# Kernel tuning notes

Hardware: AMD Instinct MI355X
Metric: run time of the kernel (lower is better)

## Reference

```python
import jax, jax.numpy as jnp
import numpy as np

B, N, D, H = 2, 2048, 512, 8
DH = D  # head_subspaces=False -> d_head = d_model
F = H * DH  # 4096, projected feature dim (RoPE applied over this full dim)


def rotate_half(x):
    # interleaved pairs (lucidrains rotary-embedding-torch default): (x0,x1)->(-x1,x0)
    x2 = x.reshape(*x.shape[:-1], -1, 2)
    return jnp.stack([-x2[..., 1], x2[..., 0]], axis=-1).reshape(x.shape)


def apply_rope(x, cos, sin):
    # x: [B,N,F], cos/sin: [N,F]
    return x * cos[None] + rotate_half(x) * sin[None]


def setup_inputs() -> dict:
    key = jax.random.key(0)
    kx, kq, kk, kv, ko = jax.random.split(key, 5)
    x = jax.random.normal(kx, (B, N, D), dtype=jnp.float32)
    # rotary tables over full projected dim, freqs repeated in interleaved pairs
    inv_freq = 1.0 / (10000.0 ** (jnp.arange(0, F, 2, dtype=jnp.float32) / F))
    freqs = jnp.arange(N, dtype=jnp.float32)[:, None] * inv_freq[None, :]  # [N, F/2]
    freqs = jnp.repeat(freqs, 2, axis=-1)  # [N, F], pairwise interleaved
    cos, sin = jnp.cos(freqs), jnp.sin(freqs)
    # causal bool mask [B, query, target] (3-dim branch of the module)
    target_mask = jnp.broadcast_to(jnp.tril(jnp.ones((N, N), dtype=bool))[None], (B, N, N))
    s = 0.02
    Wq = jax.random.normal(kq, (D, F), dtype=jnp.float32) * s
    Wk = jax.random.normal(kk, (D, F), dtype=jnp.float32) * s
    Wv = jax.random.normal(kv, (D, F), dtype=jnp.float32) * s
    bv = jnp.zeros((F,), dtype=jnp.float32)
    Wo = jax.random.normal(ko, (D, D), dtype=jnp.float32) * s
    bo = jnp.zeros((D,), dtype=jnp.float32)
    return {"x": x, "cos": cos, "sin": sin, "target_mask": target_mask,
            "Wq": Wq, "Wk": Wk, "Wv": Wv, "bv": bv, "Wo": Wo, "bo": bo}


def reference(x, cos, sin, target_mask, Wq, Wk, Wv, bv, Wo, bo):
    b, n, d = x.shape
    Q = apply_rope(x @ Wq, cos, sin)  # RoPE on full [B,N,F] projection
    K = apply_rope(x @ Wk, cos, sin)
    V = x @ Wv + bv
    # split heads: [B,H,N,DH]
    Q = Q.reshape(b, n, H, DH).transpose(0, 2, 1, 3)
    K = K.reshape(b, n, H, DH).transpose(0, 2, 1, 3)
    V = V.reshape(b, n, H, DH).transpose(0, 2, 1, 3)
    A = jnp.einsum('bhid,bhjd->bhij', Q, K)  # NOTE: no 1/sqrt(d) scaling, as in source
    A = jnp.where(target_mask[:, None, :, :], A, -jnp.inf)
    A = jax.nn.softmax(A, axis=-1)
    y = jnp.einsum('bhij,bhjd->bhid', A, V)
    # head_subspaces=False: merge heads by SUM over head axis -> [B,N,D]
    y = y.sum(axis=1)
    y = y * jax.nn.sigmoid(1.702 * y)  # QuickGELU
    return y @ Wo + bo
```

## Files before the change

kernel.cpp:

```cpp
#include <hip/hip_runtime.h>

typedef unsigned short u16;
typedef u16 u16x8 __attribute__((ext_vector_type(8)));
typedef __bf16 bf16x8 __attribute__((ext_vector_type(8)));
typedef float f32x4 __attribute__((ext_vector_type(4)));

#define DEV __device__ __forceinline__
#define MFMA16 __builtin_amdgcn_mfma_f32_16x16x32_bf16

constexpr int Bb = 2, Nctx = 2048, Dm = 512, Hh = 8, Dh = 512, Ff = 4096;
constexpr int Mrows = Bb * Nctx;

DEV float b2f(u16 u) { unsigned int i = ((unsigned int)u) << 16; return __builtin_bit_cast(float, i); }
DEV u16 f2b(float f) {
  unsigned int x = __builtin_bit_cast(unsigned int, f);
  return (u16)((x + 0x7FFFu + ((x >> 16) & 1u)) >> 16);
}
DEV bf16x8 ld8(const u16* p) { return __builtin_bit_cast(bf16x8, *(const u16x8*)p); }

DEV void gload16(const u16* g, u16* l) {
#if defined(__has_builtin) && __has_builtin(__builtin_amdgcn_global_load_lds)
  __builtin_amdgcn_global_load_lds((const __attribute__((address_space(1))) void*)(g),
                                   (__attribute__((address_space(3))) void*)(l), 16, 0, 0);
#else
  *(u16x8*)l = *(const u16x8*)g;
#endif
}

__global__ void convert_k(const float* __restrict__ in, u16* __restrict__ out, int n8) {
  int idx = blockIdx.x * 256 + threadIdx.x;
  if (idx >= n8) return;
  size_t e0 = (size_t)idx * 8;
  f32x4 a = *(const f32x4*)(in + e0);
  f32x4 b = *(const f32x4*)(in + e0 + 4);
  u16x8 o;
  #pragma unroll
  for (int i = 0; i < 4; ++i) { o[i] = f2b(a[i]); o[4 + i] = f2b(b[i]); }
  *(u16x8*)(out + e0) = o;
}

__global__ void transpose_k(const float* __restrict__ in, u16* __restrict__ out,
                            int rows, int cols) {
  __shared__ float tile[32][33];
  int bx = blockIdx.x * 32, by = blockIdx.y * 32;
  int tx = threadIdx.x, ty = threadIdx.y;
  #pragma unroll
  for (int i = ty; i < 32; i += 8)
    tile[i][tx] = in[(size_t)(by + i) * cols + bx + tx];
  __syncthreads();
  #pragma unroll
  for (int i = ty; i < 32; i += 8)
    out[(size_t)(bx + i) * rows + by + tx] = f2b(tile[tx][i]);
}

__global__ void vtrans_k(const u16* __restrict__ V, u16* __restrict__ Vt) {
  __shared__ u16 tile[32][33];
  int z = blockIdx.z;
  int b = z >> 3, h = z & 7;
  int n0 = blockIdx.x * 32, d0 = blockIdx.y * 32;
  int tx = threadIdx.x, ty = threadIdx.y;
  #pragma unroll
  for (int i = ty; i < 32; i += 8)
    tile[i][tx] = V[((size_t)(b * Nctx + n0 + i)) * Ff + h * Dh + d0 + tx];
  __syncthreads();
  #pragma unroll
  for (int i = ty; i < 32; i += 8)
    Vt[((size_t)(z * Dh + d0 + i)) * Nctx + n0 + tx] = tile[tx][i];
}

template <int MODE>
__launch_bounds__(256, 4)
__global__ void gemm2_k(const u16* __restrict__ A, const u16* __restrict__ BT,
                        void* __restrict__ Cout, const float* __restrict__ bias,
                        const float* __restrict__ cs, const float* __restrict__ sn,
                        int Ndim, int Kdim) {
  __shared__ u16 sA[128 * 32];
  __shared__ u16 sB[128 * 32];
  const int tid = threadIdx.x;
  const int wave = tid >> 6, lane = tid & 63, quad = lane >> 4, l16 = lane & 15;
  const int wy = wave >> 1, wx = wave & 1;
  const int m0 = blockIdx.y * 128, n0 = blockIdx.x * 128;
  f32x4 acc[4][4];
  #pragma unroll
  for (int i = 0; i < 4; ++i)
    #pragma unroll
    for (int j = 0; j < 4; ++j)
      #pragma unroll
      for (int r = 0; r < 4; ++r) acc[i][j][r] = 0.f;
  const int srow = tid >> 2, sch = (tid & 3) * 8;
  const u16* agp = A + (size_t)(m0 + srow) * Kdim + sch;
  const u16* bgp = BT + (size_t)(n0 + srow) * Kdim + sch;
  for (int k0 = 0; k0 < Kdim; k0 += 32) {
    __syncthreads();
    gload16(agp + k0, &sA[srow * 32 + sch]);
    gload16(agp + (size_t)64 * Kdim + k0, &sA[(64 + srow) * 32 + sch]);
    gload16(bgp + k0, &sB[srow * 32 + sch]);
    gload16(bgp + (size_t)64 * Kdim + k0, &sB[(64 + srow) * 32 + sch]);
    __syncthreads();
    bf16x8 af[4], bf[4];
    #pragma unroll
    for (int t = 0; t < 4; ++t) af[t] = ld8(&sA[(wy * 64 + t * 16 + l16) * 32 + quad * 8]);
    #pragma unroll
    for (int t = 0; t < 4; ++t) bf[t] = ld8(&sB[(wx * 64 + t * 16 + l16) * 32 + quad * 8]);
    #pragma unroll
    for (int i = 0; i < 4; ++i)
      #pragma unroll
      for (int j = 0; j < 4; ++j)
        acc[i][j] = MFMA16(af[i], bf[j], acc[i][j], 0, 0, 0);
  }
  #pragma unroll
  for (int i = 0; i < 4; ++i) {
    #pragma unroll
    for (int j = 0; j < 4; ++j) {
      int col = n0 + wx * 64 + j * 16 + l16;
      float badd = (MODE == 2 || MODE == 3) ? bias[col] : 0.f;
      #pragma unroll
      for (int r = 0; r < 4; ++r) {
        int row = m0 + wy * 64 + i * 16 + quad * 4 + r;
        float v = acc[i][j][r] + badd;
        if (MODE == 1) {
          float vp = __shfl_xor(v, 1);
          int n = row & (Nctx - 1);
          float c = cs[(size_t)n * Ff + col];
          float s = sn[(size_t)n * Ff + col];
          v = (l16 & 1) ? (v * c + vp * s) : (v * c - vp * s);
        }
        if (MODE == 3) ((float*)Cout)[(size_t)row * Ndim + col] = v;
        else           ((u16*)Cout)[(size_t)row * Ndim + col] = f2b(v);
      }
    }
  }
}

__launch_bounds__(256, 1)
__global__ void attn_k(const u16* __restrict__ Q, const u16* __restrict__ K,
                       const u16* __restrict__ Vt, u16* __restrict__ Yp) {
  __shared__ u16 sK[64 * 512];
  __shared__ u16 sP[64 * 72];
  __shared__ float sAl[64];
  __shared__ float sL[64];
  const int idx = blockIdx.x;
  const int hi = idx >> 8;
  const int bh = (idx & 7) | (hi << 3);
  const int q_ = (idx >> 3) & 31;
  const int zig = (q_ & 1) ? (31 - (q_ >> 1)) : (q_ >> 1);
  const int qt = hi ? (31 - zig) : zig;
  const int b = bh >> 3, h = bh & 7;
  const int q0 = qt * 64;
  const int wave = threadIdx.x >> 6, lane = threadIdx.x & 63;
  const int quad = lane >> 4, l16 = lane & 15;
  const int mq = q0 + wave * 16;
  const int wd = wave * 128;

  bf16x8 qf[16];
  {
    const u16* qp = Q + ((size_t)(b * Nctx + mq + l16)) * Ff + h * Dh + quad * 8;
    #pragma unroll
    for (int i = 0; i < 16; ++i) qf[i] = ld8(qp + i * 32);
  }
  f32x4 acc[4][8];
  #pragma unroll
  for (int g = 0; g < 4; ++g)
    #pragma unroll
    for (int t = 0; t < 8; ++t)
      #pragma unroll
      for (int r = 0; r < 4; ++r) acc[g][t][r] = 0.f;
  float mrun[4], lrun[4];
  #pragma unroll
  for (int r = 0; r < 4; ++r) { mrun[r] = -__builtin_inff(); lrun[r] = 0.f; }

  auto stageK = [&](int j0) {
    #pragma unroll
    for (int it = 0; it < 16; ++it) {
      int row = wave * 16 + it;
      const u16* gp = K + ((size_t)(b * Nctx + j0 + row)) * Ff + h * Dh + (((lane - row) & 63) * 8);
      gload16(gp, &sK[row * 512 + lane * 8]);
    }
  };
  const u16* vrow = Vt + ((size_t)(bh * Dh + wd + l16)) * Nctx;

  stageK(0);
  for (int jt = 0; jt <= qt; ++jt) {
    const int j0 = jt * 64;
    __syncthreads();
    f32x4 s[4];
    #pragma unroll
    for (int kg = 0; kg < 4; ++kg)
      #pragma unroll
      for (int r = 0; r < 4; ++r) s[kg][r] = 0.f;
    #pragma unroll
    for (int kk = 0; kk < 16; ++kk) {
      #pragma unroll
      for (int kg = 0; kg < 4; ++kg) {
        int key = kg * 16 + l16;
        bf16x8 bfr = ld8(&sK[key * 512 + (((kk * 4 + quad + key) & 63) * 8)]);
        s[kg] = MFMA16(qf[kk], bfr, s[kg], 0, 0, 0);
      }
    }
    const bool diag = (jt == qt);
    float p[4][4], alpha[4];
    #pragma unroll
    for (int r = 0; r < 4; ++r) {
      int qrow = mq + quad * 4 + r;
      float sv[4];
      #pragma unroll
      for (int kg = 0; kg < 4; ++kg) {
        int key = j0 + kg * 16 + l16;
        sv[kg] = (diag && key > qrow) ? -__builtin_inff() : s[kg][r];
      }
      float mx = fmaxf(fmaxf(sv[0], sv[1]), fmaxf(sv[2], sv[3]));
      mx = fmaxf(mx, __shfl_xor(mx, 1));
      mx = fmaxf(mx, __shfl_xor(mx, 2));
      mx = fmaxf(mx, __shfl_xor(mx, 4));
      mx = fmaxf(mx, __shfl_xor(mx, 8));
      float mnew = fmaxf(mrun[r], mx);
      float a = __expf(mrun[r] - mnew);
      float rs = 0.f;
      #pragma unroll
      for (int kg = 0; kg < 4; ++kg) { float pe = __expf(sv[kg] - mnew); p[r][kg] = pe; rs += pe; }
      lrun[r] = lrun[r] * a + rs;
      mrun[r] = mnew;
      alpha[r] = a;
    }
    #pragma unroll
    for (int r = 0; r < 4; ++r) {
      #pragma unroll
      for (int kg = 0; kg < 4; ++kg)
        sP[(wave * 16 + quad * 4 + r) * 72 + kg * 16 + l16] = f2b(p[r][kg]);
      if (l16 == 0) sAl[wave * 16 + quad * 4 + r] = alpha[r];
    }
    __syncthreads();
    if (jt < qt) stageK(j0 + 64);
    {
      #pragma unroll
      for (int g = 0; g < 4; ++g) {
        float a0 = sAl[g * 16 + quad * 4 + 0];
        float a1 = sAl[g * 16 + quad * 4 + 1];
        float a2 = sAl[g * 16 + quad * 4 + 2];
        float a3 = sAl[g * 16 + quad * 4 + 3];
        #pragma unroll
        for (int t = 0; t < 8; ++t) {
          acc[g][t][0] *= a0; acc[g][t][1] *= a1; acc[g][t][2] *= a2; acc[g][t][3] *= a3;
        }
      }
      bf16x8 pf[4][2];
      #pragma unroll
      for (int g = 0; g < 4; ++g)
        #pragma unroll
        for (int kk = 0; kk < 2; ++kk)
          pf[g][kk] = ld8(&sP[(g * 16 + l16) * 72 + kk * 32 + quad * 8]);
      #pragma unroll
      for (int t = 0; t < 8; ++t) {
        const u16* vp = vrow + (size_t)(t * 16) * Nctx + j0 + quad * 8;
        bf16x8 v0 = ld8(vp);
        bf16x8 v1 = ld8(vp + 32);
        #pragma unroll
        for (int g = 0; g < 4; ++g) acc[g][t] = MFMA16(pf[g][0], v0, acc[g][t], 0, 0, 0);
        #pragma unroll
        for (int g = 0; g < 4; ++g) acc[g][t] = MFMA16(pf[g][1], v1, acc[g][t], 0, 0, 0);
      }
    }
  }
  #pragma unroll
  for (int r = 0; r < 4; ++r) {
    float l = lrun[r];
    l += __shfl_xor(l, 1);
    l += __shfl_xor(l, 2);
    l += __shfl_xor(l, 4);
    l += __shfl_xor(l, 8);
    if (l16 == 0) sL[wave * 16 + quad * 4 + r] = l;
  }
  __syncthreads();
  #pragma unroll
  for (int g = 0; g < 4; ++g) {
    float inv[4];
    #pragma unroll
    for (int r = 0; r < 4; ++r) inv[r] = 1.f / sL[g * 16 + quad * 4 + r];
    #pragma unroll
    for (int t = 0; t < 8; ++t)
      #pragma unroll
      for (int r = 0; r < 4; ++r)
        Yp[((size_t)bh * Nctx + q0 + g * 16 + quad * 4 + r) * Dh + wd + t * 16 + l16] =
            f2b(acc[g][t][r] * inv[r]);
  }
}

__global__ void sumheads_k(const u16* __restrict__ Yp, u16* __restrict__ Ys) {
  size_t idx = (size_t)blockIdx.x * 256 + threadIdx.x;
  size_t e0 = idx * 8;
  int b = (int)(e0 >> 20);
  size_t rem = e0 & ((1u << 20) - 1);
  float s[8];
  #pragma unroll
  for (int e = 0; e < 8; ++e) s[e] = 0.f;
  #pragma unroll
  for (int h = 0; h < Hh; ++h) {
    u16x8 v = *(const u16x8*)&Yp[((size_t)(b * Hh + h) << 20) + rem];
    #pragma unroll
    for (int e = 0; e < 8; ++e) s[e] += b2f(v[e]);
  }
  u16x8 o;
  #pragma unroll
  for (int e = 0; e < 8; ++e) {
    float g = s[e] / (1.f + __expf(-1.702f * s[e]));
    o[e] = f2b(g);
  }
  *(u16x8*)&Ys[e0] = o;
}

extern "C" void kernel_launch(void* const* d_in, const int* in_sizes, int n_in,
                              void* d_out, int out_size, void* d_ws, size_t ws_size,
                              hipStream_t stream) {
  const float* x  = (const float*)d_in[0];
  const float* cs = (const float*)d_in[1];
  const float* sn = (const float*)d_in[2];
  int wbase = 4;
  if (n_in == 9) wbase = 3;
  if (wbase + 3 < n_in && in_sizes[wbase + 3] != 4096) wbase = (wbase == 4) ? 3 : 4;
  const float* Wq = (const float*)d_in[wbase + 0];
  const float* Wk = (const float*)d_in[wbase + 1];
  const float* Wv = (const float*)d_in[wbase + 2];
  const float* bv = (const float*)d_in[wbase + 3];
  const float* Wo = (const float*)d_in[wbase + 4];
  const float* bo = (const float*)d_in[wbase + 5];

  char* ws = (char*)d_ws;
  const size_t MiB = 1ull << 20;
  u16* WqT = (u16*)(ws + 0 * MiB);
  u16* WkT = (u16*)(ws + 4 * MiB);
  u16* WvT = (u16*)(ws + 8 * MiB);
  u16* xb  = (u16*)(ws + 12 * MiB);
  u16* Vt  = (u16*)(ws + 0 * MiB);
  u16* Qb  = (u16*)(ws + 32 * MiB);
  u16* Kb  = (u16*)(ws + 64 * MiB);
  u16* Vb  = (u16*)(ws + 96 * MiB);
  u16* Yp  = Vb;
  u16* WoT = (u16*)(ws + 128 * MiB);
  u16* Ys  = (u16*)(ws + 128 * MiB + 512 * 1024);

  dim3 tb(32, 8);
  transpose_k<<<dim3(Ff / 32, Dm / 32), tb, 0, stream>>>(Wq, WqT, Dm, Ff);
  transpose_k<<<dim3(Ff / 32, Dm / 32), tb, 0, stream>>>(Wk, WkT, Dm, Ff);
  transpose_k<<<dim3(Ff / 32, Dm / 32), tb, 0, stream>>>(Wv, WvT, Dm, Ff);
  transpose_k<<<dim3(Dm / 32, Dm / 32), tb, 0, stream>>>(Wo, WoT, Dm, Dm);
  convert_k<<<dim3(Mrows * Dm / 8 / 256), 256, 0, stream>>>(x, xb, Mrows * Dm / 8);

  gemm2_k<1><<<dim3(Ff / 128, Mrows / 128), 256, 0, stream>>>(xb, WqT, Qb, nullptr, cs, sn, Ff, Dm);
  gemm2_k<1><<<dim3(Ff / 128, Mrows / 128), 256, 0, stream>>>(xb, WkT, Kb, nullptr, cs, sn, Ff, Dm);
  gemm2_k<2><<<dim3(Ff / 128, Mrows / 128), 256, 0, stream>>>(xb, WvT, Vb, bv, nullptr, nullptr, Ff, Dm);

  vtrans_k<<<dim3(Nctx / 32, Dh / 32, Bb * Hh), tb, 0, stream>>>(Vb, Vt);

  attn_k<<<dim3(512), 256, 0, stream>>>(Qb, Kb, Vt, Yp);

  sumheads_k<<<dim3(Mrows * Dm / 8 / 256), 256, 0, stream>>>(Yp, Ys);

  gemm2_k<3><<<dim3(Dm / 128, Mrows / 128), 256, 0, stream>>>(Ys, WoT, d_out, bo, nullptr, nullptr, Dm, Dm);
}
```

Baseline: 585.6 us.

## Widen GEMM K-tile with swizzled LDS, vectorize V transpose, add MFMA priority hints

The projection GEMM now stages 64-wide K slices with an XOR-swizzled LDS layout. This halves the number of barrier pairs per tile and avoids bank conflicts on fragment reads. The V transpose kernel uses 64x64 tiles with 16-byte vector loads and stores through a swizzled shared tile in place of scalar 32x32 transposes. The attention kernel raises wave priority around its MFMA loops with s_setprio. Doubling the LDS footprint may reduce occupancy at the 4-blocks-per-CU launch bound.

```diff
diff --git a/kernel.cpp b/kernel.cpp
--- a/kernel.cpp
+++ b/kernel.cpp
@@ -54,18 +54,32 @@
 }
 
 __global__ void vtrans_k(const u16* __restrict__ V, u16* __restrict__ Vt) {
-  __shared__ u16 tile[32][33];
-  int z = blockIdx.z;
-  int b = z >> 3, h = z & 7;
-  int n0 = blockIdx.x * 32, d0 = blockIdx.y * 32;
-  int tx = threadIdx.x, ty = threadIdx.y;
-  #pragma unroll
-  for (int i = ty; i < 32; i += 8)
-    tile[i][tx] = V[((size_t)(b * Nctx + n0 + i)) * Ff + h * Dh + d0 + tx];
+  __shared__ u16 tile[64 * 64];
+  const int z = blockIdx.z;
+  const int b = z >> 3, h = z & 7;
+  const int n0 = blockIdx.x * 64, d0 = blockIdx.y * 64;
+  const int t = threadIdx.x;
+  const int nl = t >> 3;
+  const int dg = t & 7;
+  #pragma unroll
+  for (int sw = 0; sw < 2; ++sw) {
+    int n = nl + 32 * sw;
+    u16x8 v = *(const u16x8*)&V[((size_t)(b * Nctx + n0 + n)) * Ff + h * Dh + d0 + dg * 8];
+    #pragma unroll
+    for (int j = 0; j < 8; ++j) {
+      int d = dg * 8 + j;
+      int g = ((d & 7) ^ (d >> 3)) & 7;
+      tile[d * 64 + (n ^ (g << 3))] = v[j];
+    }
+  }
   __syncthreads();
   #pragma unroll
-  for (int i = ty; i < 32; i += 8)
-    Vt[((size_t)(z * Dh + d0 + i)) * Nctx + n0 + tx] = tile[tx][i];
+  for (int sw = 0; sw < 2; ++sw) {
+    int d = nl + 32 * sw;
+    int g = ((d & 7) ^ (d >> 3)) & 7;
+    u16x8 v = *(const u16x8*)&tile[d * 64 + ((dg ^ g) << 3)];
+    *(u16x8*)&Vt[((size_t)(z * Dh + d0 + d)) * Nctx + n0 + dg * 8] = v;
+  }
 }
 
 template <int MODE>
@@ -74,8 +88,8 @@
                         void* __restrict__ Cout, const float* __restrict__ bias,
                         const float* __restrict__ cs, const float* __restrict__ sn,
                         int Ndim, int Kdim) {
-  __shared__ u16 sA[128 * 32];
-  __shared__ u16 sB[128 * 32];
+  __shared__ u16 sA[128 * 64];
+  __shared__ u16 sB[128 * 64];
   const int tid = threadIdx.x;
   const int wave = tid >> 6, lane = tid & 63, quad = lane >> 4, l16 = lane & 15;
   const int wy = wave >> 1, wx = wave & 1;
@@ -87,26 +101,32 @@
     for (int j = 0; j < 4; ++j)
       #pragma unroll
       for (int r = 0; r < 4; ++r) acc[i][j][r] = 0.f;
-  const int srow = tid >> 2, sch = (tid & 3) * 8;
-  const u16* agp = A + (size_t)(m0 + srow) * Kdim + sch;
-  const u16* bgp = BT + (size_t)(n0 + srow) * Kdim + sch;
-  for (int k0 = 0; k0 < Kdim; k0 += 32) {
+  const int srow = tid >> 3;
+  const int scol = (tid & 7) * 8;
+  for (int k0 = 0; k0 < Kdim; k0 += 64) {
     __syncthreads();
-    gload16(agp + k0, &sA[srow * 32 + sch]);
-    gload16(agp + (size_t)64 * Kdim + k0, &sA[(64 + srow) * 32 + sch]);
-    gload16(bgp + k0, &sB[srow * 32 + sch]);
-    gload16(bgp + (size_t)64 * Kdim + k0, &sB[(64 + srow) * 32 + sch]);
+    #pragma unroll
+    for (int sw = 0; sw < 4; ++sw) {
+      int row = srow + 32 * sw;
+      int sc = scol ^ ((row & 7) * 8);
+      gload16(A + (size_t)(m0 + row) * Kdim + k0 + sc, &sA[row * 64 + scol]);
+      gload16(BT + (size_t)(n0 + row) * Kdim + k0 + sc, &sB[row * 64 + scol]);
+    }
     __syncthreads();
-    bf16x8 af[4], bf[4];
-    #pragma unroll
-    for (int t = 0; t < 4; ++t) af[t] = ld8(&sA[(wy * 64 + t * 16 + l16) * 32 + quad * 8]);
-    #pragma unroll
-    for (int t = 0; t < 4; ++t) bf[t] = ld8(&sB[(wx * 64 + t * 16 + l16) * 32 + quad * 8]);
-    #pragma unroll
-    for (int i = 0; i < 4; ++i)
-      #pragma unroll
-      for (int j = 0; j < 4; ++j)
-        acc[i][j] = MFMA16(af[i], bf[j], acc[i][j], 0, 0, 0);
+    #pragma unroll
+    for (int kk2 = 0; kk2 < 2; ++kk2) {
+      const int cbase = (kk2 * 32 + quad * 8) ^ ((l16 & 7) * 8);
+      bf16x8 af[4], bf[4];
+      #pragma unroll
+      for (int t = 0; t < 4; ++t) af[t] = ld8(&sA[(wy * 64 + t * 16 + l16) * 64 + cbase]);
+      #pragma unroll
+      for (int t = 0; t < 4; ++t) bf[t] = ld8(&sB[(wx * 64 + t * 16 + l16) * 64 + cbase]);
+      #pragma unroll
+      for (int i = 0; i < 4; ++i)
+        #pragma unroll
+        for (int j = 0; j < 4; ++j)
+          acc[i][j] = MFMA16(af[i], bf[j], acc[i][j], 0, 0, 0);
+    }
   }
   #pragma unroll
   for (int i = 0; i < 4; ++i) {
@@ -188,6 +208,7 @@
     for (int kg = 0; kg < 4; ++kg)
       #pragma unroll
       for (int r = 0; r < 4; ++r) s[kg][r] = 0.f;
+    __builtin_amdgcn_s_setprio(1);
     #pragma unroll
     for (int kk = 0; kk < 16; ++kk) {
       #pragma unroll
@@ -197,6 +218,7 @@
         s[kg] = MFMA16(qf[kk], bfr, s[kg], 0, 0, 0);
       }
     }
+    __builtin_amdgcn_s_setprio(0);
     const bool diag = (jt == qt);
     float p[4][4], alpha[4];
     #pragma unroll
@@ -249,6 +271,7 @@
         #pragma unroll
         for (int kk = 0; kk < 2; ++kk)
           pf[g][kk] = ld8(&sP[(g * 16 + l16) * 72 + kk * 32 + quad * 8]);
+      __builtin_amdgcn_s_setprio(1);
       #pragma unroll
       for (int t = 0; t < 8; ++t) {
         const u16* vp = vrow + (size_t)(t * 16) * Nctx + j0 + quad * 8;
@@ -259,6 +282,7 @@
         #pragma unroll
         for (int g = 0; g < 4; ++g) acc[g][t] = MFMA16(pf[g][1], v1, acc[g][t], 0, 0, 0);
       }
+      __builtin_amdgcn_s_setprio(0);
     }
   }
   #pragma unroll
@@ -349,7 +373,7 @@
   gemm2_k<1><<<dim3(Ff / 128, Mrows / 128), 256, 0, stream>>>(xb, WkT, Kb, nullptr, cs, sn, Ff, Dm);
   gemm2_k<2><<<dim3(Ff / 128, Mrows / 128), 256, 0, stream>>>(xb, WvT, Vb, bv, nullptr, nullptr, Ff, Dm);
 
-  vtrans_k<<<dim3(Nctx / 32, Dh / 32, Bb * Hh), tb, 0, stream>>>(Vb, Vt);
+  vtrans_k<<<dim3(Nctx / 64, Dh / 64, Bb * Hh), 256, 0, stream>>>(Vb, Vt);
 
   attn_k<<<dim3(512), 256, 0, stream>>>(Qb, Kb, Vt, Yp);
 
```

Measured after the change: 601.3 us. 2.7% more time.
